# Performance work log

Hardware: AMD Instinct MI355X
Metric: run time of the kernel (lower is better)

The kernel has to match this reference:

```python
import jax, jax.numpy as jnp
import numpy as np

WIDTH = 2048
NUM_HEADS = 16
HEAD_DIM = WIDTH // NUM_HEADS
BATCH = 16384


def block_diag_linear(x, w, b):
    # x: [..., width] -> [..., h, i] einsum with w: [h, i, j]
    xh = x.reshape(x.shape[:-1] + (NUM_HEADS, HEAD_DIM))
    y = jnp.einsum('...hi,hij->...hj', xh, w) + b
    return y.reshape(x.shape)


def setup_inputs() -> dict:
    key = jax.random.key(0)
    ks = jax.random.split(key, 7)
    x = jax.random.normal(ks[0], (BATCH, WIDTH), dtype=jnp.float32)
    state = jax.random.normal(ks[1], (BATCH, WIDTH), dtype=jnp.float32)
    w_in = jax.random.normal(ks[2], (NUM_HEADS, HEAD_DIM, HEAD_DIM), dtype=jnp.float32) * 0.02
    b_in = jax.random.normal(ks[3], (NUM_HEADS, HEAD_DIM), dtype=jnp.float32) * 0.02
    w_a = jax.random.normal(ks[4], (NUM_HEADS, HEAD_DIM, HEAD_DIM), dtype=jnp.float32) * 0.02
    b_a = jax.random.normal(ks[5], (NUM_HEADS, HEAD_DIM), dtype=jnp.float32) * 0.02
    a_param = jax.random.normal(ks[6], (WIDTH,), dtype=jnp.float32) * 0.5
    return {'x': x, 'state': state, 'w_in': w_in, 'b_in': b_in,
            'w_a': w_a, 'b_a': b_a, 'a_param': a_param}


def reference(x, state, w_in, b_in, w_a, b_a, a_param):
    gate_x = jax.nn.sigmoid(block_diag_linear(x, w_in, b_in))
    gate_a = jax.nn.sigmoid(block_diag_linear(x, w_a, b_a))
    log_a = -8.0 * gate_a * jax.nn.softplus(a_param)  # [B, width]
    a = jnp.exp(log_a)
    scale = jnp.sqrt(1.0 - jnp.exp(2.0 * log_a))
    return a * state + gate_x * x * scale
```

## Files before the change

kernel.cpp:

```cpp
#include <hip/hip_runtime.h>
#include <hip/hip_bf16.h>

typedef __attribute__((ext_vector_type(8))) short bf16x8;
typedef __attribute__((ext_vector_type(4))) float f32x4;
typedef __attribute__((ext_vector_type(4))) unsigned short u16x4;

#define WIDTH  2048
#define NHEADS 16
#define HDIM   128
#define BM     64

__device__ __forceinline__ unsigned short f2bf(float f) {
  union { float f; unsigned int u; } v; v.f = f;
  unsigned int u = v.u;
  unsigned int r = (u + 0x7FFFu + ((u >> 16) & 1u)) >> 16;
  return (unsigned short)r;
}

__device__ __forceinline__ float bf2f(unsigned short s) {
  union { unsigned int u; float f; } v;
  v.u = ((unsigned int)s) << 16;
  return v.f;
}

__device__ __forceinline__ unsigned int pk_bf16(float lo, float hi) {
  __hip_bfloat162 b = __float22bfloat162_rn(make_float2(lo, hi));
  union { __hip_bfloat162 b; unsigned int u; } c; c.b = b;
  return c.u;
}

#define LOG2E 1.4426950408889634f

__global__ __launch_bounds__(256) void prep_kernel(
    const float* __restrict__ w_in, const float* __restrict__ w_a,
    const float* __restrict__ a_param,
    const float* __restrict__ b_in, const float* __restrict__ b_a,
    unsigned short* __restrict__ wTin, unsigned short* __restrict__ wTa,
    float* __restrict__ sp8, float* __restrict__ sbi, float* __restrict__ sba) {
  int tid = blockIdx.x * 256 + threadIdx.x;
  int h   = tid >> 14;
  int rem = tid & 16383;
  int j   = rem >> 7;
  int i   = rem & 127;
  int src = (h << 14) + (i << 7) + j;
  wTin[tid] = f2bf(w_in[src] * LOG2E);
  wTa[tid]  = f2bf(w_a[src] * LOG2E);
  if (tid < WIDTH) {
    float v  = a_param[tid];
    float sp = (v > 20.0f) ? v : log1pf(__expf(v));
    sp8[tid] = 8.0f * sp * LOG2E;
    sbi[tid] = b_in[tid] * LOG2E;
    sba[tid] = b_a[tid] * LOG2E;
  }
}

__global__ __launch_bounds__(256, 4) void rglru_kernel(
    const float* __restrict__ x, const float* __restrict__ state,
    const float* __restrict__ sbi, const float* __restrict__ sba,
    const unsigned short* __restrict__ wTin, const unsigned short* __restrict__ wTa,
    const float* __restrict__ sp8, float* __restrict__ out) {
  __shared__ unsigned short xs[BM * HDIM];

  const int bid  = blockIdx.x;
  const int h    = bid & (NHEADS - 1);
  const int rb   = bid >> 4;
  const int t    = threadIdx.x;
  const int lane = t & 63;
  const int wid  = t >> 6;
  const int l15  = lane & 15;
  const int l4   = lane >> 4;

  const float* xtile = x + (long)rb * BM * WIDTH + h * HDIM;
#pragma unroll
  for (int it = 0; it < 8; ++it) {
    int idx = it * 256 + t;
    int r   = idx >> 5;
    int c4  = idx & 31;
    f32x4 v = __builtin_nontemporal_load(
        reinterpret_cast<const f32x4*>(xtile + (long)r * WIDTH) + c4);
    uint2 p;
    p.x = pk_bf16(v[0], v[1]);
    p.y = pk_bf16(v[2], v[3]);
    int off = (r * 256 + c4 * 8) ^ ((r & 7) << 4);
    *reinterpret_cast<uint2*>(reinterpret_cast<char*>(xs) + off) = p;
  }

  const int cb = h * HDIM + wid * 32 + l4 * 4;
  f32x4 bi0 = *reinterpret_cast<const f32x4*>(sbi + cb);
  f32x4 bi1 = *reinterpret_cast<const f32x4*>(sbi + cb + 16);
  f32x4 ba0 = *reinterpret_cast<const f32x4*>(sba + cb);
  f32x4 ba1 = *reinterpret_cast<const f32x4*>(sba + cb + 16);
  f32x4 sp0 = *reinterpret_cast<const f32x4*>(sp8 + cb);
  f32x4 sp1 = *reinterpret_cast<const f32x4*>(sp8 + cb + 16);

  __syncthreads();

  f32x4 acc_in[4][2], acc_a[4][2];
#pragma unroll
  for (int m = 0; m < 4; ++m) {
    acc_in[m][0] = bi0; acc_in[m][1] = bi1;
    acc_a[m][0]  = ba0; acc_a[m][1]  = ba1;
  }

  const unsigned short* wi0 = wTin + ((h * HDIM + wid * 32 + l15) * HDIM) + l4 * 8;
  const unsigned short* wi1 = wi0 + 16 * HDIM;
  const unsigned short* wa0 = wTa + ((h * HDIM + wid * 32 + l15) * HDIM) + l4 * 8;
  const unsigned short* wa1 = wa0 + 16 * HDIM;

  const int xsw = ((l15 & 7) << 4);

#pragma unroll
  for (int kk = 0; kk < 4; ++kk) {
    bf16x8 xfr[4];
#pragma unroll
    for (int m = 0; m < 4; ++m) {
      int boff = ((m * 16 + l15) * 256 + kk * 64 + l4 * 16) ^ xsw;
      xfr[m] = *reinterpret_cast<const bf16x8*>(
          reinterpret_cast<const char*>(xs) + boff);
    }
    bf16x8 win[2], wa[2];
    win[0] = *reinterpret_cast<const bf16x8*>(wi0 + kk * 32);
    win[1] = *reinterpret_cast<const bf16x8*>(wi1 + kk * 32);
    wa[0]  = *reinterpret_cast<const bf16x8*>(wa0 + kk * 32);
    wa[1]  = *reinterpret_cast<const bf16x8*>(wa1 + kk * 32);
#pragma unroll
    for (int m = 0; m < 4; ++m)
#pragma unroll
      for (int n = 0; n < 2; ++n) {
        acc_in[m][n] = __builtin_amdgcn_mfma_f32_16x16x32_bf16(
            win[n], xfr[m], acc_in[m][n], 0, 0, 0);
        acc_a[m][n] = __builtin_amdgcn_mfma_f32_16x16x32_bf16(
            wa[n], xfr[m], acc_a[m][n], 0, 0, 0);
      }
  }

  const long base = (long)(rb * BM + l15) * WIDTH + cb;
  const float* ps = state + base;
  float*       po = out + base;
  const char* pxs = reinterpret_cast<const char*>(xs);
  const int xe0 = (l15 * 256 + (wid * 32 + l4 * 4) * 2) ^ xsw;
  const int xe1 = (l15 * 256 + (wid * 32 + 16 + l4 * 4) * 2) ^ xsw;

#pragma unroll
  for (int m = 0; m < 4; ++m) {
#pragma unroll
    for (int n = 0; n < 2; ++n) {
      f32x4 sv = *reinterpret_cast<const f32x4*>(ps + n * 16);
      u16x4 xb = *reinterpret_cast<const u16x4*>(
          pxs + (n ? xe1 : xe0) + m * 4096);
      f32x4 sp = n ? sp1 : sp0;
      f32x4 o;
#pragma unroll
      for (int r = 0; r < 4; ++r) {
        float gx  = __builtin_amdgcn_rcpf(1.0f + exp2f(-acc_in[m][n][r]));
        float ga  = __builtin_amdgcn_rcpf(1.0f + exp2f(-acc_a[m][n][r]));
        float av  = exp2f(-ga * sp[r]);
        float sc  = sqrtf(fmaxf(1.0f - av * av, 0.0f));
        o[r] = av * sv[r] + gx * bf2f(xb[r]) * sc;
      }
      *reinterpret_cast<f32x4*>(po + n * 16) = o;
    }
    ps += 16 * WIDTH;
    po += 16 * WIDTH;
  }
}

extern "C" void kernel_launch(void* const* d_in, const int* in_sizes, int n_in,
                              void* d_out, int out_size, void* d_ws, size_t ws_size,
                              hipStream_t stream) {
  const float* x       = (const float*)d_in[0];
  const float* state   = (const float*)d_in[1];
  const float* w_in    = (const float*)d_in[2];
  const float* b_in    = (const float*)d_in[3];
  const float* w_a     = (const float*)d_in[4];
  const float* b_a     = (const float*)d_in[5];
  const float* a_param = (const float*)d_in[6];
  float* out = (float*)d_out;

  unsigned short* wTin = (unsigned short*)d_ws;
  unsigned short* wTa  = wTin + NHEADS * HDIM * HDIM;
  float*          sp8  = (float*)(wTa + NHEADS * HDIM * HDIM);
  float*          sbi  = sp8 + WIDTH;
  float*          sba  = sbi + WIDTH;

  hipLaunchKernelGGL(prep_kernel, dim3(1024), dim3(256), 0, stream,
                     w_in, w_a, a_param, b_in, b_a, wTin, wTa, sp8, sbi, sba);

  hipLaunchKernelGGL(rglru_kernel, dim3(4096), dim3(256), 0, stream,
                     x, state, sbi, sba, wTin, wTa, sp8, out);
}
```

Before: 103.0 us.

## Load x tile directly into LDS as fp32 via global_load_lds

Replaces the register-staged load/convert/store of the x tile with direct global-to-LDS DMA loads (global_load_lds, 16 bytes) that keep x as fp32 in shared memory, using an XOR swizzle on the source column. The bf16 conversion moves to the MFMA fragment reads, and the epilogue now reads x at full fp32 precision. This removes VGPR staging and conversion work in the load phase. In exchange, LDS use doubles to 32 KB per block, which may limit occupancy, and the fp32-to-bf16 packing is repeated on every fragment read.

```diff
diff --git a/kernel.cpp b/kernel.cpp
--- a/kernel.cpp
+++ b/kernel.cpp
@@ -3,7 +3,6 @@
 
 typedef __attribute__((ext_vector_type(8))) short bf16x8;
 typedef __attribute__((ext_vector_type(4))) float f32x4;
-typedef __attribute__((ext_vector_type(4))) unsigned short u16x4;
 
 #define WIDTH  2048
 #define NHEADS 16
@@ -15,12 +14,6 @@
   unsigned int u = v.u;
   unsigned int r = (u + 0x7FFFu + ((u >> 16) & 1u)) >> 16;
   return (unsigned short)r;
-}
-
-__device__ __forceinline__ float bf2f(unsigned short s) {
-  union { unsigned int u; float f; } v;
-  v.u = ((unsigned int)s) << 16;
-  return v.f;
 }
 
 __device__ __forceinline__ unsigned int pk_bf16(float lo, float hi) {
@@ -59,7 +52,7 @@
     const float* __restrict__ sbi, const float* __restrict__ sba,
     const unsigned short* __restrict__ wTin, const unsigned short* __restrict__ wTa,
     const float* __restrict__ sp8, float* __restrict__ out) {
-  __shared__ unsigned short xs[BM * HDIM];
+  __shared__ float xs[BM * HDIM];
 
   const int bid  = blockIdx.x;
   const int h    = bid & (NHEADS - 1);
@@ -70,19 +63,22 @@
   const int l15  = lane & 15;
   const int l4   = lane >> 4;
 
-  const float* xtile = x + (long)rb * BM * WIDTH + h * HDIM;
+  {
+    const float* xtile = x + (long)rb * BM * WIDTH + h * HDIM;
+    const int rloc = lane >> 5;
+    const int cc   = lane & 31;
 #pragma unroll
-  for (int it = 0; it < 8; ++it) {
-    int idx = it * 256 + t;
-    int r   = idx >> 5;
-    int c4  = idx & 31;
-    f32x4 v = __builtin_nontemporal_load(
-        reinterpret_cast<const f32x4*>(xtile + (long)r * WIDTH) + c4);
-    uint2 p;
-    p.x = pk_bf16(v[0], v[1]);
-    p.y = pk_bf16(v[2], v[3]);
-    int off = (r * 256 + c4 * 8) ^ ((r & 7) << 4);
-    *reinterpret_cast<uint2*>(reinterpret_cast<char*>(xs) + off) = p;
+    for (int i = 0; i < 8; ++i) {
+      int r    = wid * 16 + i * 2 + rloc;
+      int csrc = cc ^ ((r & 7) << 2);
+      const float* src = xtile + (long)r * WIDTH + csrc * 4;
+      unsigned lds_off = (unsigned)((wid * 16 + i * 2) * 512);
+      __builtin_amdgcn_global_load_lds(
+          (const __attribute__((address_space(1))) unsigned int*)src,
+          (__attribute__((address_space(3))) unsigned int*)(
+              (__attribute__((address_space(3))) char*)xs + lds_off),
+          16, 0, 0);
+    }
   }
 
   const int cb = h * HDIM + wid * 32 + l4 * 4;
@@ -107,16 +103,23 @@
   const unsigned short* wa0 = wTa + ((h * HDIM + wid * 32 + l15) * HDIM) + l4 * 8;
   const unsigned short* wa1 = wa0 + 16 * HDIM;
 
-  const int xsw = ((l15 & 7) << 4);
+  const char* pxs = reinterpret_cast<const char*>(xs);
 
 #pragma unroll
   for (int kk = 0; kk < 4; ++kk) {
     bf16x8 xfr[4];
 #pragma unroll
     for (int m = 0; m < 4; ++m) {
-      int boff = ((m * 16 + l15) * 256 + kk * 64 + l4 * 16) ^ xsw;
-      xfr[m] = *reinterpret_cast<const bf16x8*>(
-          reinterpret_cast<const char*>(xs) + boff);
+      int r  = m * 16 + l15;
+      int c0 = (kk * 8 + l4 * 2) ^ ((r & 7) << 2);
+      const f32x4* p = reinterpret_cast<const f32x4*>(pxs + r * 512 + c0 * 16);
+      f32x4 lo = p[0], hi = p[1];
+      union { bf16x8 v; unsigned int u[4]; } uu;
+      uu.u[0] = pk_bf16(lo[0], lo[1]);
+      uu.u[1] = pk_bf16(lo[2], lo[3]);
+      uu.u[2] = pk_bf16(hi[0], hi[1]);
+      uu.u[3] = pk_bf16(hi[2], hi[3]);
+      xfr[m] = uu.v;
     }
     bf16x8 win[2], wa[2];
     win[0] = *reinterpret_cast<const bf16x8*>(wi0 + kk * 32);
@@ -137,26 +140,25 @@
   const long base = (long)(rb * BM + l15) * WIDTH + cb;
   const float* ps = state + base;
   float*       po = out + base;
-  const char* pxs = reinterpret_cast<const char*>(xs);
-  const int xe0 = (l15 * 256 + (wid * 32 + l4 * 4) * 2) ^ xsw;
-  const int xe1 = (l15 * 256 + (wid * 32 + 16 + l4 * 4) * 2) ^ xsw;
 
 #pragma unroll
   for (int m = 0; m < 4; ++m) {
+    const int r = m * 16 + l15;
+    const int sw = (r & 7) << 2;
 #pragma unroll
     for (int n = 0; n < 2; ++n) {
       f32x4 sv = *reinterpret_cast<const f32x4*>(ps + n * 16);
-      u16x4 xb = *reinterpret_cast<const u16x4*>(
-          pxs + (n ? xe1 : xe0) + m * 4096);
+      int cx = (wid * 8 + n * 4 + l4) ^ sw;
+      f32x4 xv = *reinterpret_cast<const f32x4*>(pxs + r * 512 + cx * 16);
       f32x4 sp = n ? sp1 : sp0;
       f32x4 o;
 #pragma unroll
-      for (int r = 0; r < 4; ++r) {
-        float gx  = __builtin_amdgcn_rcpf(1.0f + exp2f(-acc_in[m][n][r]));
-        float ga  = __builtin_amdgcn_rcpf(1.0f + exp2f(-acc_a[m][n][r]));
-        float av  = exp2f(-ga * sp[r]);
+      for (int rr = 0; rr < 4; ++rr) {
+        float gx  = __builtin_amdgcn_rcpf(1.0f + exp2f(-acc_in[m][n][rr]));
+        float ga  = __builtin_amdgcn_rcpf(1.0f + exp2f(-acc_a[m][n][rr]));
+        float av  = exp2f(-ga * sp[rr]);
         float sc  = sqrtf(fmaxf(1.0f - av * av, 0.0f));
-        o[r] = av * sv[r] + gx * bf2f(xb[r]) * sc;
+        o[rr] = av * sv[rr] + gx * xv[rr] * sc;
       }
       *reinterpret_cast<f32x4*>(po + n * 16) = o;
     }
```

New measurement: 115.5 us. 1.12x slower.

## Tile weight transpose through LDS and swizzle block order across XCDs

Applied to the files above, without the earlier changes.

The prep kernel now transposes and converts the weights through a shared-memory tile. Reads become coalesced float4 loads and writes become 16-byte vector stores, replacing the strided scalar gather over 1024 blocks with 72 blocks. Separate blocks now handle the softplus and bias scaling. The main kernel remaps block IDs so that consecutive blocks on the same XCD (bid mod 8) cover contiguous row blocks and heads, which is meant to improve L2 locality. The cost is fewer prep blocks, and LDS bank conflicts in the column-wise transpose reads.

```diff
diff --git a/kernel.cpp b/kernel.cpp
--- a/kernel.cpp
+++ b/kernel.cpp
@@ -4,6 +4,7 @@
 typedef __attribute__((ext_vector_type(8))) short bf16x8;
 typedef __attribute__((ext_vector_type(4))) float f32x4;
 typedef __attribute__((ext_vector_type(4))) unsigned short u16x4;
+typedef __attribute__((ext_vector_type(8))) unsigned short u16x8;
 
 #define WIDTH  2048
 #define NHEADS 16
@@ -37,21 +38,50 @@
     const float* __restrict__ b_in, const float* __restrict__ b_a,
     unsigned short* __restrict__ wTin, unsigned short* __restrict__ wTa,
     float* __restrict__ sp8, float* __restrict__ sbi, float* __restrict__ sba) {
-  int tid = blockIdx.x * 256 + threadIdx.x;
-  int h   = tid >> 14;
-  int rem = tid & 16383;
-  int j   = rem >> 7;
-  int i   = rem & 127;
-  int src = (h << 14) + (i << 7) + j;
-  wTin[tid] = f2bf(w_in[src] * LOG2E);
-  wTa[tid]  = f2bf(w_a[src] * LOG2E);
-  if (tid < WIDTH) {
+  const int b = blockIdx.x;
+  if (b >= 64) {
+    int tid = (b - 64) * 256 + threadIdx.x;
     float v  = a_param[tid];
     float sp = (v > 20.0f) ? v : log1pf(__expf(v));
     sp8[tid] = 8.0f * sp * LOG2E;
     sbi[tid] = b_in[tid] * LOG2E;
     sba[tid] = b_a[tid] * LOG2E;
-  }
+    return;
+  }
+  const int h  = b >> 2;
+  const int i0 = (b & 3) * 32;
+  __shared__ unsigned short tl[2][32][136];
+
+  const float* s0 = w_in + h * 16384 + i0 * 128;
+  const float* s1 = w_a  + h * 16384 + i0 * 128;
+#pragma unroll
+  for (int it = 0; it < 4; ++it) {
+    int e = it * 1024 + threadIdx.x * 4;
+    int r = e >> 7, c = e & 127;
+    f32x4 v0 = *reinterpret_cast<const f32x4*>(s0 + r * 128 + c);
+    f32x4 v1 = *reinterpret_cast<const f32x4*>(s1 + r * 128 + c);
+#pragma unroll
+    for (int k = 0; k < 4; ++k) {
+      tl[0][r][c + k] = f2bf(v0[k] * LOG2E);
+      tl[1][r][c + k] = f2bf(v1[k] * LOG2E);
+    }
+  }
+  __syncthreads();
+
+  const int j  = threadIdx.x >> 1;
+  const int ih = (threadIdx.x & 1) * 16;
+  u16x8 o0a, o0b, o1a, o1b;
+#pragma unroll
+  for (int k = 0; k < 8; ++k) {
+    o0a[k] = tl[0][ih + k][j];      o0b[k] = tl[0][ih + 8 + k][j];
+    o1a[k] = tl[1][ih + k][j];      o1b[k] = tl[1][ih + 8 + k][j];
+  }
+  unsigned short* d0 = wTin + h * 16384 + j * 128 + i0 + ih;
+  unsigned short* d1 = wTa  + h * 16384 + j * 128 + i0 + ih;
+  *reinterpret_cast<u16x8*>(d0)     = o0a;
+  *reinterpret_cast<u16x8*>(d0 + 8) = o0b;
+  *reinterpret_cast<u16x8*>(d1)     = o1a;
+  *reinterpret_cast<u16x8*>(d1 + 8) = o1b;
 }
 
 __global__ __launch_bounds__(256, 4) void rglru_kernel(
@@ -61,7 +91,8 @@
     const float* __restrict__ sp8, float* __restrict__ out) {
   __shared__ unsigned short xs[BM * HDIM];
 
-  const int bid  = blockIdx.x;
+  const int bid0 = blockIdx.x;
+  const int bid  = ((bid0 & 7) << 9) + (bid0 >> 3);
   const int h    = bid & (NHEADS - 1);
   const int rb   = bid >> 4;
   const int t    = threadIdx.x;
@@ -183,7 +214,7 @@
   float*          sbi  = sp8 + WIDTH;
   float*          sba  = sbi + WIDTH;
 
-  hipLaunchKernelGGL(prep_kernel, dim3(1024), dim3(256), 0, stream,
+  hipLaunchKernelGGL(prep_kernel, dim3(72), dim3(256), 0, stream,
                      w_in, w_a, a_param, b_in, b_a, wTin, wTa, sp8, sbi, sba);
 
   hipLaunchKernelGGL(rglru_kernel, dim3(4096), dim3(256), 0, stream,
```

After: 104.9 us. Within noise of the previous version (+1.9%).
